# Optimization experiments

Measured on AMD Instinct MI355X. Metric: run time of the kernel, lower is better.

The kernel has to match this reference:

```python
import jax, jax.numpy as jnp
import numpy as np
import math

D_MODEL = 256
PRED_LEN = 256
K = 32
LOW_FREQ = 1


def setup_inputs() -> dict:
    key = jax.random.key(0)
    x = jax.random.normal(key, (8, 1024, D_MODEL), dtype=jnp.float32)
    return {"x": x}


def reference(x):
    """x: (b, t, d) -> reconstructed/extrapolated series (b, t+pred_len, d)."""
    b, t, d = x.shape
    k_ = K  # K < t//2, so the explicit-k branch of the torch module is taken

    x_freq = jnp.fft.rfft(x, axis=1)  # (b, t//2+1, d) complex
    if t % 2 == 0:
        x_freq_high = x_freq[:, LOW_FREQ:-1]  # drop DC..low_freq-1 and Nyquist
    else:
        x_freq_high = x_freq[:, LOW_FREQ:]

    # top-k magnitudes over the frequency axis, independently per (b, d)
    mag = jnp.abs(x_freq_high)                                   # (b, F, d)
    _, idx = jax.lax.top_k(jnp.transpose(mag, (0, 2, 1)), k_)    # (b, d, k)
    idx = jnp.transpose(idx, (0, 2, 1)) + LOW_FREQ               # (b, k, d) into x_freq

    x_freq_topk = jnp.take_along_axis(x_freq, idx, axis=1)       # (b, k, d) complex
    freqs = jnp.fft.rfftfreq(t).astype(x.dtype)                  # (t//2+1,)
    f_topk = freqs[idx]                                          # (b, k, d)

    # append conjugate / negative-frequency pair for a real reconstruction
    x_ext = jnp.concatenate([x_freq_topk, jnp.conj(x_freq_topk)], axis=1)  # (b, 2k, d)
    f_ext = jnp.concatenate([f_topk, -f_topk], axis=1)                     # (b, 2k, d)

    t_val = jnp.arange(t + PRED_LEN, dtype=x.dtype)              # (T,)
    amp = (jnp.abs(x_ext) / t)[:, :, None, :]                    # (b, 2k, 1, d)
    phase = jnp.angle(x_ext)[:, :, None, :]                      # (b, 2k, 1, d)
    arg = (2.0 * math.pi) * f_ext[:, :, None, :] * t_val[None, None, :, None] + phase
    x_time = amp * jnp.cos(arg)                                  # (b, 2k, T, d)
    return jnp.sum(x_time, axis=1)                               # (b, T, d)
```

## Files before the change

kernel.cpp:

```cpp
#include <hip/hip_runtime.h>
#include <math.h>

#define T_LEN 1024
#define PRED_LEN 256
#define OUT_T (T_LEN + PRED_LEN)
#define DM 256
#define KSEL 32
#define RTAU 1e-4f

#define PAD16(i) ((i) + ((i) >> 4))

__device__ __constant__ float W16RF[16] = {
    1.0f,  0.92387953f,  0.70710678f,  0.38268343f, 0.0f, -0.38268343f, -0.70710678f, -0.92387953f,
   -1.0f, -0.92387953f, -0.70710678f, -0.38268343f, 0.0f,  0.38268343f,  0.70710678f,  0.92387953f };
__device__ __constant__ float W16IF[16] = {
    0.0f, -0.38268343f, -0.70710678f, -0.92387953f, -1.0f, -0.92387953f, -0.70710678f, -0.38268343f,
    0.0f,  0.38268343f,  0.70710678f,  0.92387953f,  1.0f,  0.92387953f,  0.70710678f,  0.38268343f };

__global__ void fl_twiddle_kernel(double* __restrict__ gwr, double* __restrict__ gwi,
                                  float2* __restrict__ gwF) {
    int e = blockIdx.x * 64 + threadIdx.x;
    double ang = (double)e * (6.283185307179586476925286766559 / 1024.0);
    double c = cos(ang), s = -sin(ang);
    gwr[e] = c; gwi[e] = s;
    gwF[e] = float2{ (float)c, (float)s };
}

__device__ __forceinline__ void fft1024(const float2* __restrict__ xin,
                                        const float2* __restrict__ twF,
                                        int lane, int w, float* ar, float* ai) {
    float Fr[4][4], Fi[4][4];
#pragma unroll
    for (int n1a = 0; n1a < 4; ++n1a) {
        float2 a  = xin[lane + 64 * (n1a + 0)];
        float2 bb = xin[lane + 64 * (n1a + 4)];
        float2 cV = xin[lane + 64 * (n1a + 8)];
        float2 d  = xin[lane + 64 * (n1a + 12)];
        float t0r = a.x + cV.x, t0i = a.y + cV.y;
        float t1r = a.x - cV.x, t1i = a.y - cV.y;
        float t2r = bb.x + d.x, t2i = bb.y + d.y;
        float t3r = bb.x - d.x, t3i = bb.y - d.y;
        Fr[n1a][0] = t0r + t2r;  Fi[n1a][0] = t0i + t2i;
        Fr[n1a][2] = t0r - t2r;  Fi[n1a][2] = t0i - t2i;
        Fr[n1a][1] = t1r + t3i;  Fi[n1a][1] = t1i - t3r;
        Fr[n1a][3] = t1r - t3i;  Fi[n1a][3] = t1i + t3r;
    }
#pragma unroll
    for (int q = 0; q < 4; ++q) {
        const int k1 = (w << 2) | q;
        float cr = Fr[0][q], ci = Fi[0][q];
#pragma unroll
        for (int n1a = 1; n1a < 4; ++n1a) {
            int e = (n1a * k1) & 15;
            float wr = W16RF[e], wi = W16IF[e];
            cr += Fr[n1a][q] * wr - Fi[n1a][q] * wi;
            ci += Fr[n1a][q] * wi + Fi[n1a][q] * wr;
        }
        float2 tw = twF[PAD16((lane * k1) & 1023)];
        ar[q] = cr * tw.x - ci * tw.y;
        ai[q] = cr * tw.y + ci * tw.x;
    }
#pragma unroll
    for (int s = 0; s < 6; ++s) {
        const int half = 32 >> s;
        const int e = (lane & (half - 1)) << s;
        float2 tw = twF[PAD16(e << 4)];
        const bool up = (lane & half) != 0;
#pragma unroll
        for (int q = 0; q < 4; ++q) {
            float orr = __shfl_xor(ar[q], half);
            float oii = __shfl_xor(ai[q], half);
            float sr = ar[q] + orr, si = ai[q] + oii;
            float dr = orr - ar[q], di = oii - ai[q];
            ar[q] = up ? (dr * tw.x - di * tw.y) : sr;
            ai[q] = up ? (dr * tw.y + di * tw.x) : si;
        }
    }
}

__global__ void __launch_bounds__(256, 4)
fl_fused_kernel(const float* __restrict__ x,
                const double* __restrict__ gwr, const double* __restrict__ gwi,
                const float2* __restrict__ gwF, float* __restrict__ out) {
    __shared__ float2 twF[PAD16(1023) + 1];
    __shared__ float2 spP[PAD16(1023) + 1];
    __shared__ char smemU[8192];
    __shared__ unsigned selw[64];
    float2* xsh  = (float2*)smemU;
    float*  mg   = (float*)smemU;
    int*    hist = (int*)(smemU + 4096);

    const int tid  = threadIdx.x;
    const int lane = tid & 63;
    const int w    = tid >> 6;

    const int bid = blockIdx.x;
    const int sp  = ((bid & 7) << 7) | (bid >> 3);
    const int b   = sp >> 7;
    const int d0  = (sp & 127) << 1;

    for (int j = 0; j < 4; ++j) {
        int e = tid + (j << 8);
        twF[PAD16(e)] = gwF[e];
        xsh[e] = *reinterpret_cast<const float2*>(&x[(((size_t)(b << 10) + e) << 8) + d0]);
    }
    if (tid < 64) selw[tid] = 0u;
    __syncthreads();

    float ar[4], ai[4];
    fft1024(xsh, twF, lane, w, ar, ai);

    const int krev = (int)(__brev((unsigned)lane) >> 26);
#pragma unroll
    for (int q = 0; q < 4; ++q) {
        int k = ((w << 2) | q) + (krev << 4);
        spP[PAD16(k)] = float2{ ar[q], ai[q] };
    }
    __syncthreads();

#pragma unroll
    for (int h = 0; h < 2; ++h) {
        int m = tid + (h << 8);
        int n = (1024 - m) & 1023;
        float2 Pk = spP[PAD16(m)];
        float2 Pn = spP[PAD16(n)];
        float rr0 = 0.5f * (Pk.x + Pn.x), ii0 = 0.5f * (Pk.y - Pn.y);
        float rr1 = 0.5f * (Pk.y + Pn.y), ii1 = 0.5f * (Pn.x - Pk.x);
        mg[m]       = rr0 * rr0 + ii0 * ii0;
        mg[512 + m] = rr1 * rr1 + ii1 * ii1;
    }
    __syncthreads();

    if (tid < 128) {
        const int c = tid >> 6;
        const float* mgc = mg + (c << 9);
        int* histc = hist + (c << 8);

        float v[8]; int hiw[8];
#pragma unroll
        for (int q = 0; q < 8; ++q) v[q] = mgc[(q << 6) | lane];
        if (lane == 0) v[0] = -1.0f;
#pragma unroll
        for (int q = 0; q < 8; ++q) hiw[q] = __float_as_int(v[q]);

        int mx = hiw[0];
#pragma unroll
        for (int q = 1; q < 8; ++q) mx = max(mx, hiw[q]);
#pragma unroll
        for (int off = 1; off < 64; off <<= 1) mx = max(mx, __shfl_xor(mx, off));

        const int base = (mx >> 20) - 250;
        int idx[8];
#pragma unroll
        for (int q = 0; q < 8; ++q) {
            int t = (hiw[q] >> 20) - base;
            idx[q] = t < 0 ? 0 : t;
        }

        *reinterpret_cast<int4*>(&histc[lane << 2]) = int4{0, 0, 0, 0};
#pragma unroll
        for (int q = 0; q < 8; ++q) atomicAdd(&histc[idx[q]], 1);

        int4 cc = *reinterpret_cast<int4*>(&histc[lane << 2]);
        int s_local = cc.x + cc.y + cc.z + cc.w;

        int s = s_local;
#pragma unroll
        for (int off = 1; off < 64; off <<= 1) {
            int t = __shfl_down(s, off);
            if (lane + off < 64) s += t;
        }
        const int S_gt = s - s_local;
        const int A3 = S_gt;
        const int A2 = A3 + cc.w;
        const int A1 = A2 + cc.z;
        const int A0 = A1 + cc.y;

        int foundB = -1, foundR = 0;
        if (A0 < KSEL && A0 + cc.x >= KSEL) { foundB = (lane << 2) | 0; foundR = KSEL - A0; }
        if (A1 < KSEL && A1 + cc.y >= KSEL) { foundB = (lane << 2) | 1; foundR = KSEL - A1; }
        if (A2 < KSEL && A2 + cc.z >= KSEL) { foundB = (lane << 2) | 2; foundR = KSEL - A2; }
        if (A3 < KSEL && A3 + cc.w >= KSEL) { foundB = (lane << 2) | 3; foundR = KSEL - A3; }

        unsigned long long fm = __ballot(foundB >= 0);
        const int srcB = (int)(__ffsll((unsigned long long)fm) - 1);
        const int B = __shfl(foundB, srcB);
        const int r = __shfl(foundR, srcB);

        unsigned selmask = 0, candmask = 0;
#pragma unroll
        for (int q = 0; q < 8; ++q) {
            if (idx[q] > B) selmask |= (1u << q);
            else if (idx[q] == B) candmask |= (1u << q);
        }

        for (int it = 0; it < r; ++it) {
            float bv = -2.0f; int bq = -1;
#pragma unroll
            for (int q = 0; q < 8; ++q) {
                bool cand = ((candmask >> q) & 1u) != 0;
                if (cand && v[q] > bv) { bv = v[q]; bq = q; }
            }
            int bi = (bq < 0) ? 0x7FFFFFFF : ((bq << 6) | lane);
#pragma unroll
            for (int off = 1; off < 64; off <<= 1) {
                float ov = __shfl_xor(bv, off);
                int   oi = __shfl_xor(bi, off);
                if (ov > bv || (ov == bv && oi < bi)) { bv = ov; bi = oi; }
            }
            if (bi != 0x7FFFFFFF && lane == (bi & 63)) {
                unsigned bit = 1u << (bi >> 6);
                selmask  |= bit;
                candmask &= ~bit;
            }
        }

        {
            float vminS = 3.0e38f, vmaxU = -3.0e38f;
#pragma unroll
            for (int q = 0; q < 8; ++q) {
                if ((selmask >> q) & 1u) vminS = fminf(vminS, v[q]);
                else                     vmaxU = fmaxf(vmaxU, v[q]);
            }
#pragma unroll
            for (int off = 1; off < 64; off <<= 1) {
                vminS = fminf(vminS, __shfl_xor(vminS, off));
                vmaxU = fmaxf(vmaxU, __shfl_xor(vmaxU, off));
            }
            const float tau = RTAU * vminS;
            if (vminS - vmaxU < tau) {
                const float lo = vmaxU - tau, hi = vminS + tau;
                unsigned candq = 0; int nAbove = 0;
#pragma unroll
                for (int q = 0; q < 8; ++q) {
                    bool inw = (v[q] >= lo) && (v[q] <= hi);
                    if (inw) candq |= (1u << q);
                    if (((selmask >> q) & 1u) && v[q] > hi) ++nAbove;
                }
#pragma unroll
                for (int off = 1; off < 64; off <<= 1) nAbove += __shfl_xor(nAbove, off);
                const int kneed = KSEL - nAbove;
                selmask &= ~candq;

                const float* xcol = x + ((size_t)(b << 10) << 8) + d0 + c;
                double sV = -1.0; int sSrc = 0; int cnum = 0;
                for (int q = 0; q < 8; ++q) {
                    unsigned long long bal = __ballot((candq >> q) & 1u);
                    while (bal) {
                        int srcl = (int)(__ffsll(bal) - 1);
                        bal &= bal - 1;
                        int m = (q << 6) | srcl;
                        double sr = 0.0, si = 0.0;
                        for (int u = 0; u < 16; ++u) {
                            int n = lane + (u << 6);
                            double xvd = (double)xcol[(size_t)n << 8];
                            int e = (m * n) & 1023;
                            sr = fma(xvd, gwr[e], sr);
                            si = fma(xvd, gwi[e], si);
                        }
#pragma unroll
                        for (int off = 1; off < 64; off <<= 1) {
                            sr += __shfl_xor(sr, off);
                            si += __shfl_xor(si, off);
                        }
                        if (lane == cnum) { sV = sr * sr + si * si; sSrc = (q << 6) | srcl; }
                        ++cnum;
                        if (cnum >= 64) break;
                    }
                    if (cnum >= 64) break;
                }
                for (int it = 0; it < kneed; ++it) {
                    double bv = sV; int bl = lane;
#pragma unroll
                    for (int off = 1; off < 64; off <<= 1) {
                        double ov = __shfl_xor(bv, off);
                        int    ol = __shfl_xor(bl, off);
                        if (ov > bv || (ov == bv && ol < bl)) { bv = ov; bl = ol; }
                    }
                    int wsrc = __shfl(sSrc, bl);
                    if (lane == (wsrc & 63)) selmask |= 1u << (wsrc >> 6);
                    if (lane == bl) sV = -2.0;
                }
            }
        }

#pragma unroll
        for (int q = 0; q < 8; ++q) {
            if ((selmask >> q) & 1u) {
                int m  = (q << 6) | lane;
                int mm = 1024 - m;
                atomicOr(&selw[(c << 5) | (m  >> 5)], 1u << (m  & 31));
                atomicOr(&selw[(c << 5) | (mm >> 5)], 1u << (mm & 31));
            }
        }
    }
    __syncthreads();

    {
        float2* zc = (float2*)smemU;
#pragma unroll
        for (int jj = 0; jj < 4; ++jj) {
            int k = tid + (jj << 8);
            int n = (1024 - k) & 1023;
            float2 Pk = spP[PAD16(k)];
            float2 Pn = spP[PAD16(n)];
            float X0r = 0.5f * (Pk.x + Pn.x), X0i = 0.5f * (Pk.y - Pn.y);
            float X1r = 0.5f * (Pk.y + Pn.y), X1i = 0.5f * (Pn.x - Pk.x);
            bool s0 = (selw[(k >> 5)]      >> (k & 31)) & 1u;
            bool s1 = (selw[32 + (k >> 5)] >> (k & 31)) & 1u;
            float Zr = (s0 ? X0r : 0.0f) - (s1 ? X1i : 0.0f);
            float Zi = (s0 ? X0i : 0.0f) + (s1 ? X1r : 0.0f);
            zc[k] = float2{ Zr, -Zi };
        }
    }
    __syncthreads();

    fft1024(xsh, twF, lane, w, ar, ai);

    {
        const float S = 1.0f / 1024.0f;
        float2* o2 = reinterpret_cast<float2*>(out + (size_t)b * OUT_T * DM + d0);
#pragma unroll
        for (int q = 0; q < 4; ++q) {
            int t = ((w << 2) | q) + (krev << 4);
            float2 o{ ar[q] * S, -ai[q] * S };
            o2[(size_t)t * 128] = o;
            if (t < PRED_LEN) o2[(size_t)(t + T_LEN) * 128] = o;
        }
    }
}

extern "C" void kernel_launch(void* const* d_in, const int* in_sizes, int n_in,
                              void* d_out, int out_size, void* d_ws, size_t ws_size,
                              hipStream_t stream) {
    const float* x = (const float*)d_in[0];
    float* out = (float*)d_out;

    char* w = (char*)d_ws;
    double* gwr = (double*)(w);
    double* gwi = (double*)(w + 1024 * sizeof(double));
    float2* gwF = (float2*)(w + 2048 * sizeof(double));

    hipLaunchKernelGGL(fl_twiddle_kernel, dim3(16), dim3(64), 0, stream, gwr, gwi, gwF);
    hipLaunchKernelGGL(fl_fused_kernel, dim3(1024), dim3(256), 0, stream,
                       x, gwr, gwi, gwF, out);
}
```

Baseline: 42.76 us.

## Fuse magnitude computation into top-k and overlap spectrum unpack with selection

Removes the separate magnitude pass and its barrier. The two selection wavefronts now compute magnitudes directly from the packed spectrum. The other two wavefronts unpack the two real spectra into shared memory while selection runs. The synthesis spectrum is built from the half-spectrum using conjugate symmetry, with a halved selection bitmask, and written into the padded spP buffer so the inverse FFT reads a padded layout. This costs an extra pass and barrier to build the Z array and uses more shared memory for the separate histogram.

New measurement: 40.81 us. 4.6% less time.

```diff
diff --git a/kernel.cpp b/kernel.cpp
--- a/kernel.cpp
+++ b/kernel.cpp
@@ -26,16 +26,21 @@
     gwF[e] = float2{ (float)c, (float)s };
 }
 
+template<bool PADDED>
 __device__ __forceinline__ void fft1024(const float2* __restrict__ xin,
                                         const float2* __restrict__ twF,
                                         int lane, int w, float* ar, float* ai) {
     float Fr[4][4], Fi[4][4];
 #pragma unroll
     for (int n1a = 0; n1a < 4; ++n1a) {
-        float2 a  = xin[lane + 64 * (n1a + 0)];
-        float2 bb = xin[lane + 64 * (n1a + 4)];
-        float2 cV = xin[lane + 64 * (n1a + 8)];
-        float2 d  = xin[lane + 64 * (n1a + 12)];
+        int i0 = lane + 64 * (n1a + 0);
+        int i1 = lane + 64 * (n1a + 4);
+        int i2 = lane + 64 * (n1a + 8);
+        int i3 = lane + 64 * (n1a + 12);
+        float2 a  = xin[PADDED ? PAD16(i0) : i0];
+        float2 bb = xin[PADDED ? PAD16(i1) : i1];
+        float2 cV = xin[PADDED ? PAD16(i2) : i2];
+        float2 d  = xin[PADDED ? PAD16(i3) : i3];
         float t0r = a.x + cV.x, t0i = a.y + cV.y;
         float t1r = a.x - cV.x, t1i = a.y - cV.y;
         float t2r = bb.x + d.x, t2i = bb.y + d.y;
@@ -85,10 +90,10 @@
     __shared__ float2 twF[PAD16(1023) + 1];
     __shared__ float2 spP[PAD16(1023) + 1];
     __shared__ char smemU[8192];
-    __shared__ unsigned selw[64];
+    __shared__ int hist[512];
+    __shared__ unsigned selw[32];
     float2* xsh  = (float2*)smemU;
-    float*  mg   = (float*)smemU;
-    int*    hist = (int*)(smemU + 4096);
+    float2* xunp = (float2*)smemU;
 
     const int tid  = threadIdx.x;
     const int lane = tid & 63;
@@ -104,11 +109,11 @@
         twF[PAD16(e)] = gwF[e];
         xsh[e] = *reinterpret_cast<const float2*>(&x[(((size_t)(b << 10) + e) << 8) + d0]);
     }
-    if (tid < 64) selw[tid] = 0u;
+    if (tid < 32) selw[tid] = 0u;
     __syncthreads();
 
     float ar[4], ai[4];
-    fft1024(xsh, twF, lane, w, ar, ai);
+    fft1024<false>(xsh, twF, lane, w, ar, ai);
 
     const int krev = (int)(__brev((unsigned)lane) >> 26);
 #pragma unroll
@@ -118,27 +123,22 @@
     }
     __syncthreads();
 
-#pragma unroll
-    for (int h = 0; h < 2; ++h) {
-        int m = tid + (h << 8);
-        int n = (1024 - m) & 1023;
-        float2 Pk = spP[PAD16(m)];
-        float2 Pn = spP[PAD16(n)];
-        float rr0 = 0.5f * (Pk.x + Pn.x), ii0 = 0.5f * (Pk.y - Pn.y);
-        float rr1 = 0.5f * (Pk.y + Pn.y), ii1 = 0.5f * (Pn.x - Pk.x);
-        mg[m]       = rr0 * rr0 + ii0 * ii0;
-        mg[512 + m] = rr1 * rr1 + ii1 * ii1;
-    }
-    __syncthreads();
-
     if (tid < 128) {
         const int c = tid >> 6;
-        const float* mgc = mg + (c << 9);
         int* histc = hist + (c << 8);
 
         float v[8]; int hiw[8];
 #pragma unroll
-        for (int q = 0; q < 8; ++q) v[q] = mgc[(q << 6) | lane];
+        for (int q = 0; q < 8; ++q) {
+            int m = (q << 6) | lane;
+            int n = (1024 - m) & 1023;
+            float2 Pk = spP[PAD16(m)];
+            float2 Pn = spP[PAD16(n)];
+            float rr, ii;
+            if (c == 0) { rr = 0.5f * (Pk.x + Pn.x); ii = 0.5f * (Pk.y - Pn.y); }
+            else        { rr = 0.5f * (Pk.y + Pn.y); ii = 0.5f * (Pn.x - Pk.x); }
+            v[q] = rr * rr + ii * ii;
+        }
         if (lane == 0) v[0] = -1.0f;
 #pragma unroll
         for (int q = 0; q < 8; ++q) hiw[q] = __float_as_int(v[q]);
@@ -287,35 +287,45 @@
 #pragma unroll
         for (int q = 0; q < 8; ++q) {
             if ((selmask >> q) & 1u) {
-                int m  = (q << 6) | lane;
-                int mm = 1024 - m;
-                atomicOr(&selw[(c << 5) | (m  >> 5)], 1u << (m  & 31));
-                atomicOr(&selw[(c << 5) | (mm >> 5)], 1u << (mm & 31));
-            }
-        }
-    }
-    __syncthreads();
-
-    {
-        float2* zc = (float2*)smemU;
-#pragma unroll
-        for (int jj = 0; jj < 4; ++jj) {
-            int k = tid + (jj << 8);
+                int m = (q << 6) | lane;
+                atomicOr(&selw[(c << 4) | (m >> 5)], 1u << (m & 31));
+            }
+        }
+    } else {
+        const int t2 = tid - 128;
+#pragma unroll
+        for (int j = 0; j < 4; ++j) {
+            int k = t2 + (j << 7);
             int n = (1024 - k) & 1023;
             float2 Pk = spP[PAD16(k)];
             float2 Pn = spP[PAD16(n)];
-            float X0r = 0.5f * (Pk.x + Pn.x), X0i = 0.5f * (Pk.y - Pn.y);
-            float X1r = 0.5f * (Pk.y + Pn.y), X1i = 0.5f * (Pn.x - Pk.x);
-            bool s0 = (selw[(k >> 5)]      >> (k & 31)) & 1u;
-            bool s1 = (selw[32 + (k >> 5)] >> (k & 31)) & 1u;
-            float Zr = (s0 ? X0r : 0.0f) - (s1 ? X1i : 0.0f);
-            float Zi = (s0 ? X0i : 0.0f) + (s1 ? X1r : 0.0f);
-            zc[k] = float2{ Zr, -Zi };
+            xunp[k]       = float2{ 0.5f * (Pk.x + Pn.x), 0.5f * (Pk.y - Pn.y) };
+            xunp[512 + k] = float2{ 0.5f * (Pk.y + Pn.y), 0.5f * (Pn.x - Pk.x) };
         }
     }
     __syncthreads();
 
-    fft1024(xsh, twF, lane, w, ar, ai);
+#pragma unroll
+    for (int jj = 0; jj < 4; ++jj) {
+        int k = tid + (jj << 8);
+        float2 z{ 0.0f, 0.0f };
+        if (k != 0 && k != 512) {
+            int fold = (k < 512) ? k : (1024 - k);
+            float sgn = (k < 512) ? 1.0f : -1.0f;
+            float2 X0 = xunp[fold];
+            float2 X1 = xunp[512 + fold];
+            X0.y *= sgn; X1.y *= sgn;
+            bool s0 = (selw[fold >> 5]        >> (fold & 31)) & 1u;
+            bool s1 = (selw[16 + (fold >> 5)] >> (fold & 31)) & 1u;
+            float Zr = (s0 ? X0.x : 0.0f) - (s1 ? X1.y : 0.0f);
+            float Zi = (s0 ? X0.y : 0.0f) + (s1 ? X1.x : 0.0f);
+            z = float2{ Zr, -Zi };
+        }
+        spP[PAD16(k)] = z;
+    }
+    __syncthreads();
+
+    fft1024<true>(spP, twF, lane, w, ar, ai);
 
     {
         const float S = 1.0f / 1024.0f;
```
